# Kernel optimization log

Hardware: AMD Instinct MI355X
Metric: run time of the kernel (lower is better)

Reference implementation:

```python
import jax, jax.numpy as jnp
import numpy as np

N_HEAD = 12

def setup_inputs() -> dict:
    key = jax.random.key(0)
    ks = jax.random.split(key, 5)
    B, T, C = 4, 2048, 768
    x = jax.random.normal(ks[0], (B, T, C), dtype=jnp.float32)
    s_in = 1.0 / np.sqrt(C)
    W_qkv = jax.random.normal(ks[1], (C, 3 * C), dtype=jnp.float32) * s_in
    b_qkv = jnp.zeros((3 * C,), dtype=jnp.float32)
    W_proj = jax.random.normal(ks[2], (C, C), dtype=jnp.float32) * s_in
    b_proj = jnp.zeros((C,), dtype=jnp.float32)
    return {"x": x, "W_qkv": W_qkv, "b_qkv": b_qkv, "W_proj": W_proj, "b_proj": b_proj}


def reference(x, W_qkv, b_qkv, W_proj, b_proj):
    B, T, C = x.shape
    H = N_HEAD
    D = C // H  # head dim
    qkv = x @ W_qkv + b_qkv                      # [B,T,3C]
    q, k, v = jnp.split(qkv, 3, axis=-1)
    # [B,T,C] -> [B,H,T,D]
    q = q.reshape(B, T, H, D).transpose(0, 2, 1, 3)
    k = k.reshape(B, T, H, D).transpose(0, 2, 1, 3)
    v = v.reshape(B, T, H, D).transpose(0, 2, 1, 3)
    att = jnp.einsum("bhqd,bhkd->bhqk", q, k) / jnp.sqrt(jnp.asarray(D, x.dtype))
    causal = jnp.tril(jnp.ones((T, T), dtype=bool))
    att = jnp.where(causal, att, jnp.asarray(-jnp.inf, att.dtype))
    att = jax.nn.softmax(att, axis=-1)
    y = jnp.einsum("bhqk,bhkd->bhqd", att, v)    # [B,H,T,D]
    y = y.transpose(0, 2, 1, 3).reshape(B, T, C)
    return y @ W_proj + b_proj
```

## Files before the change

### kernel.cpp

```cpp
#include <hip/hip_runtime.h>
#include <hip/hip_bf16.h>

typedef __bf16 bf16x8 __attribute__((ext_vector_type(8)));
typedef float f32x4 __attribute__((ext_vector_type(4)));
typedef unsigned int u32x4 __attribute__((ext_vector_type(4)));
typedef unsigned int u32x2 __attribute__((ext_vector_type(2)));
typedef int i32x2 __attribute__((ext_vector_type(2)));
typedef unsigned short u16;
typedef unsigned long long u64;

#define WAITVM(n) asm volatile("s_waitcnt vmcnt(" #n ")" ::: "memory")
#define SBAR() asm volatile("s_barrier" ::: "memory")

__device__ __forceinline__ u16 f2bf(float f) {
  unsigned u = __builtin_bit_cast(unsigned, f);
  u += 0x7FFFu + ((u >> 16) & 1u);
  return (u16)(u >> 16);
}
__device__ __forceinline__ unsigned cvtpk(float a, float b) {
  float2 f; f.x = a; f.y = b;
  __hip_bfloat162 h = __float22bfloat162_rn(f);
  unsigned u;
  __builtin_memcpy(&u, &h, 4);
  return u;
}

__device__ __forceinline__ void plswap(unsigned &a, unsigned &b) {
  i32x2 r = __builtin_amdgcn_permlane32_swap((int)a, (int)b, false, false);
  a = (unsigned)r[0];
  b = (unsigned)r[1];
}

__device__ __forceinline__ void gll16(const u16* g, u16* l) {
  __builtin_amdgcn_global_load_lds(
      (const __attribute__((address_space(1))) unsigned int*)g,
      (__attribute__((address_space(3))) unsigned int*)l, 16, 0, 0);
}

__global__ void cast_x_kernel(const float* __restrict__ in, u16* __restrict__ out, int n4) {
  int i = blockIdx.x * blockDim.x + threadIdx.x;
  if (i >= n4) return;
  f32x4 v = *(const f32x4*)(in + (size_t)i * 4);
  u32x2 pk;
  pk[0] = cvtpk(v[0], v[1]);
  pk[1] = cvtpk(v[2], v[3]);
  *(u32x2*)(out + (size_t)i * 4) = pk;
}

__global__ void transpose_cast_kernel(const float* __restrict__ W, u16* __restrict__ WT, int K, int N) {
  __shared__ float tile[32][33];
  int c0 = blockIdx.x * 32, r0 = blockIdx.y * 32;
  int tx = threadIdx.x & 31, tg = threadIdx.x >> 5;
#pragma unroll
  for (int i = 0; i < 4; ++i) {
    int r = tg + i * 8;
    tile[r][tx] = W[(size_t)(r0 + r) * N + c0 + tx];
  }
  __syncthreads();
#pragma unroll
  for (int i = 0; i < 4; ++i) {
    int r = tg + i * 8;
    WT[(size_t)(c0 + r) * K + r0 + tx] = f2bf(tile[tx][r]);
  }
}

__global__ __launch_bounds__(256, 4) void gemm_qkv_kernel(
    const u16* __restrict__ A, const u16* __restrict__ BT, const float* __restrict__ bias,
    u16* __restrict__ Qb, u16* __restrict__ Kb, u16* __restrict__ Vt) {
  constexpr int K = 768;
  constexpr int NS = K / 32;
  __shared__ u16 Asm[2][128 * 32];
  __shared__ u16 Bsm[2][128 * 32];
  const int tid = threadIdx.x;
  const int w = tid >> 6, lane = tid & 63;
  const int l15 = lane & 15, quad = lane >> 4;
  const int srow = tid >> 2, scol = (tid & 3) * 8;
  const int m0 = blockIdx.y * 128, n0 = blockIdx.x * 128;
  const u16* Ag = A + (size_t)(m0 + srow) * K + scol;
  const u16* Bg = BT + (size_t)(n0 + srow) * K + scol;
  const int mw = (w >> 1) * 64, nw = (w & 1) * 64;
  f32x4 acc[4][4];
#pragma unroll
  for (int i = 0; i < 4; ++i)
#pragma unroll
    for (int j = 0; j < 4; ++j) acc[i][j] = {0.f, 0.f, 0.f, 0.f};

  auto STAGE = [&](int buf, int ks) {
    const u16* a = Ag + ks * 32;
    const u16* b = Bg + ks * 32;
#pragma unroll
    for (int rb = 0; rb < 2; ++rb) {
      gll16(a + (size_t)rb * 64 * K, &Asm[buf][(rb * 64 + w * 16) * 32]);
      gll16(b + (size_t)rb * 64 * K, &Bsm[buf][(rb * 64 + w * 16) * 32]);
    }
  };
  auto COMPUTE = [&](int buf) {
    bf16x8 af[4], bfj[4];
#pragma unroll
    for (int i = 0; i < 4; ++i) af[i] = *(const bf16x8*)&Asm[buf][(mw + i * 16 + l15) * 32 + quad * 8];
#pragma unroll
    for (int j = 0; j < 4; ++j) bfj[j] = *(const bf16x8*)&Bsm[buf][(nw + j * 16 + l15) * 32 + quad * 8];
#pragma unroll
    for (int i = 0; i < 4; ++i)
#pragma unroll
      for (int j = 0; j < 4; ++j)
        acc[i][j] = __builtin_amdgcn_mfma_f32_16x16x32_bf16(af[i], bfj[j], acc[i][j], 0, 0, 0);
  };

  STAGE(0, 0);
  for (int s = 0; s + 2 < NS; s += 2) {
    STAGE(1, s + 1); WAITVM(4); SBAR(); COMPUTE(0); SBAR();
    STAGE(0, s + 2); WAITVM(4); SBAR(); COMPUTE(1); SBAR();
  }
  STAGE(1, NS - 1); WAITVM(4); SBAR(); COMPUTE(0);
  WAITVM(0); SBAR(); COMPUTE(1);

  const int sec = blockIdx.x / 6;
  const int nbase = n0 - sec * 768;
#pragma unroll
  for (int j = 0; j < 4; ++j) {
    const int nloc = nbase + nw + j * 16 + l15;
    const float bv = bias[sec * 768 + nloc];
    const int h = nloc >> 6, d = nloc & 63;
#pragma unroll
    for (int i = 0; i < 4; ++i) {
      const int m = m0 + mw + i * 16 + quad * 4;
      const int bb = m >> 11, trow = m & 2047;
      if (sec == 2) {
        u32x2 pk;
        pk[0] = cvtpk(acc[i][j][0] + bv, acc[i][j][1] + bv);
        pk[1] = cvtpk(acc[i][j][2] + bv, acc[i][j][3] + bv);
        *(u32x2*)(Vt + (size_t)((bb * 12 + h) * 64 + d) * 2048 + trow) = pk;
      } else {
        u16* dst = (sec == 0) ? Qb : Kb;
        const float scl = (sec == 0) ? 0.125f * 1.44269504f : 1.0f;
#pragma unroll
        for (int r = 0; r < 4; ++r)
          dst[(size_t)((bb * 12 + h) * 2048 + trow + r) * 64 + d] = f2bf((acc[i][j][r] + bv) * scl);
      }
    }
  }
}

__global__ __launch_bounds__(256, 4) void gemm_proj_kernel(
    const u16* __restrict__ A, const u16* __restrict__ BT, const float* __restrict__ bias,
    float* __restrict__ out) {
  constexpr int K = 768;
  constexpr int NS = K / 32;
  __shared__ u16 Asm[2][64 * 32];
  __shared__ u16 Bsm[2][128 * 32];
  const int tid = threadIdx.x;
  const int w = tid >> 6, lane = tid & 63;
  const int l15 = lane & 15, quad = lane >> 4;
  const int srow = tid >> 2, scol = (tid & 3) * 8;
  const int m0 = blockIdx.y * 64, n0 = blockIdx.x * 128;
  const u16* Ag = A + (size_t)(m0 + srow) * K + scol;
  const u16* Bg = BT + (size_t)(n0 + srow) * K + scol;
  const int mw = (w >> 1) * 32, nw = (w & 1) * 64;
  f32x4 acc[2][4];
#pragma unroll
  for (int i = 0; i < 2; ++i)
#pragma unroll
    for (int j = 0; j < 4; ++j) acc[i][j] = {0.f, 0.f, 0.f, 0.f};

  auto STAGE = [&](int buf, int ks) {
    const u16* a = Ag + ks * 32;
    const u16* b = Bg + ks * 32;
    gll16(a, &Asm[buf][(w * 16) * 32]);
#pragma unroll
    for (int rb = 0; rb < 2; ++rb)
      gll16(b + (size_t)rb * 64 * K, &Bsm[buf][(rb * 64 + w * 16) * 32]);
  };
  auto COMPUTE = [&](int buf) {
    bf16x8 af[2], bfj[4];
#pragma unroll
    for (int i = 0; i < 2; ++i) af[i] = *(const bf16x8*)&Asm[buf][(mw + i * 16 + l15) * 32 + quad * 8];
#pragma unroll
    for (int j = 0; j < 4; ++j) bfj[j] = *(const bf16x8*)&Bsm[buf][(nw + j * 16 + l15) * 32 + quad * 8];
#pragma unroll
    for (int i = 0; i < 2; ++i)
#pragma unroll
      for (int j = 0; j < 4; ++j)
        acc[i][j] = __builtin_amdgcn_mfma_f32_16x16x32_bf16(af[i], bfj[j], acc[i][j], 0, 0, 0);
  };

  STAGE(0, 0);
  for (int s = 0; s + 2 < NS; s += 2) {
    STAGE(1, s + 1); WAITVM(3); SBAR(); COMPUTE(0); SBAR();
    STAGE(0, s + 2); WAITVM(3); SBAR(); COMPUTE(1); SBAR();
  }
  STAGE(1, NS - 1); WAITVM(3); SBAR(); COMPUTE(0);
  WAITVM(0); SBAR(); COMPUTE(1);

#pragma unroll
  for (int j = 0; j < 4; ++j) {
    const int n = n0 + nw + j * 16 + l15;
    const float bv = bias[n];
#pragma unroll
    for (int i = 0; i < 2; ++i) {
      const int m = m0 + mw + i * 16 + quad * 4;
#pragma unroll
      for (int r = 0; r < 4; ++r) out[(size_t)(m + r) * 768 + n] = acc[i][j][r] + bv;
    }
  }
}

__global__ __launch_bounds__(256) void attn_split_kernel(
    const u16* __restrict__ Qg, const u16* __restrict__ Kg, const u16* __restrict__ Vtg,
    u16* __restrict__ Yb, float* __restrict__ Opart, float* __restrict__ lpart) {
  constexpr int T = 2048, D = 64;
  constexpr int LDP = 72;
  constexpr float MBOUND = 20.0f;
  __shared__ u16 Ks[64 * LDP];
  __shared__ u16 VTs[64 * LDP];
  const int s = 79 - blockIdx.x;
  const int bh = blockIdx.y;
  int qt, c;
  if (s < 8) { qt = s; c = 0; }
  else if (s < 24) { qt = 8 + ((s - 8) >> 1); c = (s - 8) & 1; }
  else if (s < 48) { int u = s - 24; int q3 = u / 3; qt = 16 + q3; c = u - 3 * q3; }
  else { int u = s - 48; qt = 24 + (u >> 2); c = u & 3; }
  const int niter = min(8, qt + 1 - 8 * c);
  const int tid = threadIdx.x;
  const int w = tid >> 6, lane = tid & 63;
  const int l15 = lane & 15, quad = lane >> 4;
  const int srow = tid >> 2, scol = (tid & 3) * 16;
  const u16* Kp = Kg + (size_t)bh * T * D;
  const u16* VTp = Vtg + (size_t)bh * D * T;

  const int qq = qt * 64 + w * 16 + l15;
  const u16* qrow = Qg + ((size_t)bh * T + qq) * D;
  const bf16x8 qfa = *(const bf16x8*)(qrow + quad * 8);
  const bf16x8 qfb = *(const bf16x8*)(qrow + 32 + quad * 8);

  f32x4 o[4] = {{0,0,0,0},{0,0,0,0},{0,0,0,0},{0,0,0,0}};
  float lv = 0.f;

  int ktg = c * 8;
  u32x4 kA = *(const u32x4*)(Kp + (size_t)(ktg * 64 + srow) * D + scol);
  u32x4 kB = *(const u32x4*)(Kp + (size_t)(ktg * 64 + srow) * D + scol + 8);
  u32x4 vA = *(const u32x4*)(VTp + (size_t)srow * T + ktg * 64 + scol);
  u32x4 vB = *(const u32x4*)(VTp + (size_t)srow * T + ktg * 64 + scol + 8);

  for (int j = 0; j < niter; ++j) {
    ktg = c * 8 + j;
    __syncthreads();
    *(u32x4*)&Ks[srow * LDP + scol] = kA;
    *(u32x4*)&Ks[srow * LDP + scol + 8] = kB;
    {
      u32x2 t0; t0[0] = vA[0]; t0[1] = vA[1];
      u32x2 t1; t1[0] = vA[2]; t1[1] = vA[3];
      u32x2 t2; t2[0] = vB[0]; t2[1] = vB[1];
      u32x2 t3; t3[0] = vB[2]; t3[1] = vB[3];
      *(u32x2*)&VTs[srow * LDP + scol] = t0;
      *(u32x2*)&VTs[srow * LDP + scol + 8] = t1;
      *(u32x2*)&VTs[srow * LDP + scol + 4] = t2;
      *(u32x2*)&VTs[srow * LDP + scol + 12] = t3;
    }
    __syncthreads();
    if (j + 1 < niter) {
      const int k1 = (ktg + 1) * 64;
      kA = *(const u32x4*)(Kp + (size_t)(k1 + srow) * D + scol);
      kB = *(const u32x4*)(Kp + (size_t)(k1 + srow) * D + scol + 8);
      vA = *(const u32x4*)(VTp + (size_t)srow * T + k1 + scol);
      vB = *(const u32x4*)(VTp + (size_t)srow * T + k1 + scol + 8);
    }
    f32x4 sA[4];
#pragma unroll
    for (int t = 0; t < 4; ++t) sA[t] = {-MBOUND, -MBOUND, -MBOUND, -MBOUND};
#pragma unroll
    for (int t = 0; t < 4; ++t) {
      const bf16x8 kf0 = *(const bf16x8*)&Ks[(t * 16 + l15) * LDP + quad * 8];
      const bf16x8 kf1 = *(const bf16x8*)&Ks[(t * 16 + l15) * LDP + 32 + quad * 8];
      sA[t] = __builtin_amdgcn_mfma_f32_16x16x32_bf16(kf0, qfa, sA[t], 0, 0, 0);
      sA[t] = __builtin_amdgcn_mfma_f32_16x16x32_bf16(kf1, qfb, sA[t], 0, 0, 0);
    }
    if (ktg == qt) {
      const int k0 = ktg * 64;
#pragma unroll
      for (int t = 0; t < 4; ++t)
#pragma unroll
        for (int r = 0; r < 4; ++r)
          if (k0 + t * 16 + quad * 4 + r > qq) sA[t][r] = -1e30f;
    }
    unsigned W[4][2];
#pragma unroll
    for (int t = 0; t < 4; ++t) {
      float e0 = __builtin_amdgcn_exp2f(sA[t][0]);
      float e1 = __builtin_amdgcn_exp2f(sA[t][1]);
      float e2 = __builtin_amdgcn_exp2f(sA[t][2]);
      float e3 = __builtin_amdgcn_exp2f(sA[t][3]);
      lv += (e0 + e1) + (e2 + e3);
      W[t][0] = cvtpk(e0, e1);
      W[t][1] = cvtpk(e2, e3);
    }
    plswap(W[0][0], W[1][0]);
    plswap(W[0][1], W[1][1]);
    plswap(W[2][0], W[3][0]);
    plswap(W[2][1], W[3][1]);
    u32x4 paw; paw[0] = W[0][0]; paw[1] = W[0][1]; paw[2] = W[1][0]; paw[3] = W[1][1];
    u32x4 pbw; pbw[0] = W[2][0]; pbw[1] = W[2][1]; pbw[2] = W[3][0]; pbw[3] = W[3][1];
    const bf16x8 pa = __builtin_bit_cast(bf16x8, paw);
    const bf16x8 pb = __builtin_bit_cast(bf16x8, pbw);
#pragma unroll
    for (int t = 0; t < 4; ++t) {
      const bf16x8 vf0 = *(const bf16x8*)&VTs[(t * 16 + l15) * LDP + quad * 8];
      const bf16x8 vf1 = *(const bf16x8*)&VTs[(t * 16 + l15) * LDP + 32 + quad * 8];
      o[t] = __builtin_amdgcn_mfma_f32_16x16x32_bf16(vf0, pa, o[t], 0, 0, 0);
      o[t] = __builtin_amdgcn_mfma_f32_16x16x32_bf16(vf1, pb, o[t], 0, 0, 0);
    }
  }
  lv += __shfl_xor(lv, 16);
  lv += __shfl_xor(lv, 32);
  if (qt <= 7) {
    const float inv = 1.f / lv;
    const int bidx = bh / 12, hidx = bh % 12;
    u16* y = Yb + ((size_t)bidx * T + qq) * 768 + hidx * 64;
#pragma unroll
    for (int t = 0; t < 4; ++t) {
      u32x2 pk;
      pk[0] = cvtpk(o[t][0] * inv, o[t][1] * inv);
      pk[1] = cvtpk(o[t][2] * inv, o[t][3] * inv);
      *(u32x2*)(y + t * 16 + quad * 4) = pk;
    }
  } else {
    const size_t pidx = (size_t)bh * 80 + s;
    float* Op = Opart + pidx * 4096 + (size_t)(w * 16 + l15) * 64;
#pragma unroll
    for (int t = 0; t < 4; ++t) *(f32x4*)(Op + t * 16 + quad * 4) = o[t];
    if (quad == 0) lpart[pidx * 64 + w * 16 + l15] = lv;
  }
}

__global__ __launch_bounds__(256) void attn_combine_kernel(
    const float* __restrict__ Opart, const float* __restrict__ lpart, u16* __restrict__ Yb) {
  constexpr int T = 2048;
  const int qt = 8 + blockIdx.x;
  const int bh = blockIdx.y;
  const int nch = (qt < 16) ? 2 : (qt < 24) ? 3 : 4;
  const int off = (qt < 16) ? 8 + (qt - 8) * 2 : (qt < 24) ? 24 + (qt - 16) * 3 : 48 + (qt - 24) * 4;
  const size_t base = (size_t)bh * 80 + off;
  const int tid = threadIdx.x;
  const int q = tid >> 2, db = (tid & 3) * 16;
  f32x4 o[4] = {{0,0,0,0},{0,0,0,0},{0,0,0,0},{0,0,0,0}};
  float l = 0.f;
  for (int cc = 0; cc < nch; ++cc) {
    const float* Op = Opart + (base + cc) * 4096 + (size_t)q * 64 + db;
#pragma unroll
    for (int v = 0; v < 4; ++v) o[v] += *(const f32x4*)(Op + v * 4);
    l += lpart[(base + cc) * 64 + q];
  }
  const float inv = 1.f / l;
  const int bidx = bh / 12, hidx = bh % 12;
  u16* y = Yb + ((size_t)bidx * T + qt * 64 + q) * 768 + hidx * 64 + db;
  u32x4 pk;
  pk[0] = cvtpk(o[0][0] * inv, o[0][1] * inv);
  pk[1] = cvtpk(o[0][2] * inv, o[0][3] * inv);
  pk[2] = cvtpk(o[1][0] * inv, o[1][1] * inv);
  pk[3] = cvtpk(o[1][2] * inv, o[1][3] * inv);
  *(u32x4*)y = pk;
  pk[0] = cvtpk(o[2][0] * inv, o[2][1] * inv);
  pk[1] = cvtpk(o[2][2] * inv, o[2][3] * inv);
  pk[2] = cvtpk(o[3][0] * inv, o[3][1] * inv);
  pk[3] = cvtpk(o[3][2] * inv, o[3][3] * inv);
  *(u32x4*)(y + 8) = pk;
}

__global__ __launch_bounds__(256) void attn_kernel(
    const u16* __restrict__ Qg, const u16* __restrict__ Kg, const u16* __restrict__ Vtg,
    u16* __restrict__ Yb) {
  constexpr int T = 2048, D = 64;
  constexpr int LDP = 72;
  constexpr float MBOUND = 20.0f;
  __shared__ u16 Ks[64 * LDP];
  __shared__ u16 VTs[64 * LDP];
  __shared__ u16 Ps[4 * 32 * LDP];
  const int qb = 15 - blockIdx.x;
  const int bh = blockIdx.y;
  const int Q0 = qb * 128;
  const int bidx = bh / 12, hidx = bh % 12;
  const int tid = threadIdx.x;
  const int w = tid >> 6, lane = tid & 63;
  const int l15 = lane & 15, quad = lane >> 4;
  const int srow = tid >> 2, scol = (tid & 3) * 16;
  const u16* Kp = Kg + (size_t)bh * T * D;
  const u16* VTp = Vtg + (size_t)bh * D * T;
  u16* pw0 = &Ps[(w * 32) * LDP];
  u16* pw1 = &Ps[(w * 32 + 16) * LDP];
  const u16* qrow0 = Qg + ((size_t)bh * T + Q0 + w * 16 + l15) * D;
  const bf16x8 qf0a = *(const bf16x8*)(qrow0 + quad * 8);
  const bf16x8 qf0b = *(const bf16x8*)(qrow0 + 32 + quad * 8);
  const bf16x8 qf1a = *(const bf16x8*)(qrow0 + (size_t)64 * D + quad * 8);
  const bf16x8 qf1b = *(const bf16x8*)(qrow0 + (size_t)64 * D + 32 + quad * 8);
  const int qq0 = Q0 + w * 16 + l15, qq1 = qq0 + 64;
  f32x4 o0[4] = {{0,0,0,0},{0,0,0,0},{0,0,0,0},{0,0,0,0}};
  f32x4 o1[4] = {{0,0,0,0},{0,0,0,0},{0,0,0,0},{0,0,0,0}};
  float l0v = 0.f, l1v = 0.f;
  const int nkt = 2 * qb + 2;
  u32x4 kA = *(const u32x4*)(Kp + (size_t)srow * D + scol);
  u32x4 kB = *(const u32x4*)(Kp + (size_t)srow * D + scol + 8);
  u32x4 vA = *(const u32x4*)(VTp + (size_t)srow * T + scol);
  u32x4 vB = *(const u32x4*)(VTp + (size_t)srow * T + scol + 8);
  for (int kt = 0; kt < nkt; ++kt) {
    __syncthreads();
    *(u32x4*)&Ks[srow * LDP + scol] = kA;
    *(u32x4*)&Ks[srow * LDP + scol + 8] = kB;
    *(u32x4*)&VTs[srow * LDP + scol] = vA;
    *(u32x4*)&VTs[srow * LDP + scol + 8] = vB;
    __syncthreads();
    if (kt + 1 < nkt) {
      const int k1 = (kt + 1) * 64;
      kA = *(const u32x4*)(Kp + (size_t)(k1 + srow) * D + scol);
      kB = *(const u32x4*)(Kp + (size_t)(k1 + srow) * D + scol + 8);
      vA = *(const u32x4*)(VTp + (size_t)srow * T + k1 + scol);
      vB = *(const u32x4*)(VTp + (size_t)srow * T + k1 + scol + 8);
    }
    const int k0 = kt * 64;
    const bool g0a = (kt <= 2 * qb);
    f32x4 s0[4] = {{0,0,0,0},{0,0,0,0},{0,0,0,0},{0,0,0,0}};
    f32x4 s1[4] = {{0,0,0,0},{0,0,0,0},{0,0,0,0},{0,0,0,0}};
#pragma unroll
    for (int t = 0; t < 4; ++t) {
      const bf16x8 kf0 = *(const bf16x8*)&Ks[(t * 16 + l15) * LDP + quad * 8];
      const bf16x8 kf1 = *(const bf16x8*)&Ks[(t * 16 + l15) * LDP + 32 + quad * 8];
      s0[t] = __builtin_amdgcn_mfma_f32_16x16x32_bf16(kf0, qf0a, s0[t], 0, 0, 0);
      s0[t] = __builtin_amdgcn_mfma_f32_16x16x32_bf16(kf1, qf0b, s0[t], 0, 0, 0);
      s1[t] = __builtin_amdgcn_mfma_f32_16x16x32_bf16(kf0, qf1a, s1[t], 0, 0, 0);
      s1[t] = __builtin_amdgcn_mfma_f32_16x16x32_bf16(kf1, qf1b, s1[t], 0, 0, 0);
    }
    if (g0a) {
      if (kt == 2 * qb) {
#pragma unroll
        for (int t = 0; t < 4; ++t)
#pragma unroll
          for (int r = 0; r < 4; ++r)
            if (k0 + t * 16 + quad * 4 + r > qq0) s0[t][r] = -1e30f;
      }
#pragma unroll
      for (int t = 0; t < 4; ++t) {
        float e0 = __builtin_amdgcn_exp2f(s0[t][0] - MBOUND);
        float e1 = __builtin_amdgcn_exp2f(s0[t][1] - MBOUND);
        float e2 = __builtin_amdgcn_exp2f(s0[t][2] - MBOUND);
        float e3 = __builtin_amdgcn_exp2f(s0[t][3] - MBOUND);
        l0v += (e0 + e1) + (e2 + e3);
        u32x2 pk;
        pk[0] = cvtpk(e0, e1);
        pk[1] = cvtpk(e2, e3);
        *(u32x2*)&pw0[l15 * LDP + t * 16 + quad * 4] = pk;
      }
    }
    {
      if (kt == 2 * qb + 1) {
#pragma unroll
        for (int t = 0; t < 4; ++t)
#pragma unroll
          for (int r = 0; r < 4; ++r)
            if (k0 + t * 16 + quad * 4 + r > qq1) s1[t][r] = -1e30f;
      }
#pragma unroll
      for (int t = 0; t < 4; ++t) {
        float e0 = __builtin_amdgcn_exp2f(s1[t][0] - MBOUND);
        float e1 = __builtin_amdgcn_exp2f(s1[t][1] - MBOUND);
        float e2 = __builtin_amdgcn_exp2f(s1[t][2] - MBOUND);
        float e3 = __builtin_amdgcn_exp2f(s1[t][3] - MBOUND);
        l1v += (e0 + e1) + (e2 + e3);
        u32x2 pk;
        pk[0] = cvtpk(e0, e1);
        pk[1] = cvtpk(e2, e3);
        *(u32x2*)&pw1[l15 * LDP + t * 16 + quad * 4] = pk;
      }
    }
    const bf16x8 p0a = *(const bf16x8*)&pw0[l15 * LDP + quad * 8];
    const bf16x8 p0b = *(const bf16x8*)&pw0[l15 * LDP + 32 + quad * 8];
    const bf16x8 p1a = *(const bf16x8*)&pw1[l15 * LDP + quad * 8];
    const bf16x8 p1b = *(const bf16x8*)&pw1[l15 * LDP + 32 + quad * 8];
#pragma unroll
    for (int t = 0; t < 4; ++t) {
      const bf16x8 vf0 = *(const bf16x8*)&VTs[(t * 16 + l15) * LDP + quad * 8];
      const bf16x8 vf1 = *(const bf16x8*)&VTs[(t * 16 + l15) * LDP + 32 + quad * 8];
      if (g0a) {
        o0[t] = __builtin_amdgcn_mfma_f32_16x16x32_bf16(vf0, p0a, o0[t], 0, 0, 0);
        o0[t] = __builtin_amdgcn_mfma_f32_16x16x32_bf16(vf1, p0b, o0[t], 0, 0, 0);
      }
      o1[t] = __builtin_amdgcn_mfma_f32_16x16x32_bf16(vf0, p1a, o1[t], 0, 0, 0);
      o1[t] = __builtin_amdgcn_mfma_f32_16x16x32_bf16(vf1, p1b, o1[t], 0, 0, 0);
    }
  }
  l0v += __shfl_xor(l0v, 16); l0v += __shfl_xor(l0v, 32);
  l1v += __shfl_xor(l1v, 16); l1v += __shfl_xor(l1v, 32);
  const float inv0 = 1.f / l0v, inv1 = 1.f / l1v;
  u16* y0 = Yb + ((size_t)bidx * T + qq0) * 768 + hidx * 64;
  u16* y1 = Yb + ((size_t)bidx * T + qq1) * 768 + hidx * 64;
#pragma unroll
  for (int t = 0; t < 4; ++t) {
    u32x2 pk0, pk1;
    pk0[0] = cvtpk(o0[t][0] * inv0, o0[t][1] * inv0);
    pk0[1] = cvtpk(o0[t][2] * inv0, o0[t][3] * inv0);
    pk1[0] = cvtpk(o1[t][0] * inv1, o1[t][1] * inv1);
    pk1[1] = cvtpk(o1[t][2] * inv1, o1[t][3] * inv1);
    *(u32x2*)(y0 + t * 16 + quad * 4) = pk0;
    *(u32x2*)(y1 + t * 16 + quad * 4) = pk1;
  }
}

extern "C" void kernel_launch(void* const* d_in, const int* in_sizes, int n_in,
                              void* d_out, int out_size, void* d_ws, size_t ws_size,
                              hipStream_t stream) {
  const float* x = (const float*)d_in[0];
  const float* W_qkv = (const float*)d_in[1];
  const float* b_qkv = (const float*)d_in[2];
  const float* W_proj = (const float*)d_in[3];
  const float* b_proj = (const float*)d_in[4];
  float* out = (float*)d_out;

  constexpr size_t MC = (size_t)8192 * 768;
  u16* xb = (u16*)d_ws;
  u16* Qb = xb + MC;
  u16* Kb = Qb + MC;
  u16* Vt = Kb + MC;
  u16* Yb = Vt + MC;
  u16* WqkvT = Yb + MC;
  u16* WprojT = WqkvT + (size_t)2304 * 768;
  constexpr size_t BASE_U16 = 5 * MC + (size_t)2304 * 768 + (size_t)768 * 768;
  float* Opart = (float*)((u16*)d_ws + BASE_U16);
  float* lpart = Opart + (size_t)3840 * 4096;
  constexpr size_t NEED = BASE_U16 * 2 + ((size_t)3840 * 4096 + (size_t)3840 * 64) * 4;
  const bool use_split = (ws_size >= NEED);

  cast_x_kernel<<<6291456 / (4 * 256), 256, 0, stream>>>(x, xb, 6291456 / 4);
  transpose_cast_kernel<<<dim3(2304 / 32, 768 / 32), 256, 0, stream>>>(W_qkv, WqkvT, 768, 2304);
  transpose_cast_kernel<<<dim3(768 / 32, 768 / 32), 256, 0, stream>>>(W_proj, WprojT, 768, 768);
  gemm_qkv_kernel<<<dim3(18, 64), 256, 0, stream>>>(xb, WqkvT, b_qkv, Qb, Kb, Vt);
  if (use_split) {
    attn_split_kernel<<<dim3(80, 48), 256, 0, stream>>>(Qb, Kb, Vt, Yb, Opart, lpart);
    attn_combine_kernel<<<dim3(24, 48), 256, 0, stream>>>(Opart, lpart, Yb);
  } else {
    attn_kernel<<<dim3(16, 48), 256, 0, stream>>>(Qb, Kb, Vt, Yb);
  }
  gemm_proj_kernel<<<dim3(6, 128), 256, 0, stream>>>(Yb, WprojT, b_proj, out);
}
```

Measured before the change: 229.2 us.

## Process two query tiles per split attention block to reuse K/V loads

Each split-attention block now handles 128 query rows (two 64-row tiles) and shares every K/V tile staged in LDS between both, halving K/V global traffic and LDS staging per query. The grid, partial buffers and combine kernel are rebuilt around 128-row tiles, and the combine kernel now handles 128 rows per block. s_setprio hints are added around the MFMA sections. In exchange the grid has half as many blocks, register pressure rises from two accumulator sets, and the first tile does masked or skipped work on the diagonal iterations.

After: 238.5 us. +4.0%, slower.

```diff
diff --git a/kernel.cpp b/kernel.cpp
--- a/kernel.cpp
+++ b/kernel.cpp
@@ -213,14 +213,15 @@
   constexpr float MBOUND = 20.0f;
   __shared__ u16 Ks[64 * LDP];
   __shared__ u16 VTs[64 * LDP];
-  const int s = 79 - blockIdx.x;
+  const int s = 39 - blockIdx.x;
   const int bh = blockIdx.y;
-  int qt, c;
-  if (s < 8) { qt = s; c = 0; }
-  else if (s < 24) { qt = 8 + ((s - 8) >> 1); c = (s - 8) & 1; }
-  else if (s < 48) { int u = s - 24; int q3 = u / 3; qt = 16 + q3; c = u - 3 * q3; }
-  else { int u = s - 48; qt = 24 + (u >> 2); c = u & 3; }
-  const int niter = min(8, qt + 1 - 8 * c);
+  int qt2, c;
+  if (s < 4) { qt2 = s; c = 0; }
+  else if (s < 12) { qt2 = 4 + ((s - 4) >> 1); c = (s - 4) & 1; }
+  else if (s < 24) { int u = s - 12; int q3 = u / 3; qt2 = 8 + q3; c = u - 3 * q3; }
+  else { int u = s - 24; qt2 = 12 + (u >> 2); c = u & 3; }
+  const int nkt = 2 * qt2 + 2;
+  const int niter = min(8, nkt - 8 * c);
   const int tid = threadIdx.x;
   const int w = tid >> 6, lane = tid & 63;
   const int l15 = lane & 15, quad = lane >> 4;
@@ -228,13 +229,17 @@
   const u16* Kp = Kg + (size_t)bh * T * D;
   const u16* VTp = Vtg + (size_t)bh * D * T;
 
-  const int qq = qt * 64 + w * 16 + l15;
-  const u16* qrow = Qg + ((size_t)bh * T + qq) * D;
-  const bf16x8 qfa = *(const bf16x8*)(qrow + quad * 8);
-  const bf16x8 qfb = *(const bf16x8*)(qrow + 32 + quad * 8);
-
-  f32x4 o[4] = {{0,0,0,0},{0,0,0,0},{0,0,0,0},{0,0,0,0}};
-  float lv = 0.f;
+  const int Q0 = qt2 * 128;
+  const int qq0 = Q0 + w * 16 + l15, qq1 = qq0 + 64;
+  const u16* qrow = Qg + ((size_t)bh * T + qq0) * D;
+  const bf16x8 qf0a = *(const bf16x8*)(qrow + quad * 8);
+  const bf16x8 qf0b = *(const bf16x8*)(qrow + 32 + quad * 8);
+  const bf16x8 qf1a = *(const bf16x8*)(qrow + (size_t)64 * D + quad * 8);
+  const bf16x8 qf1b = *(const bf16x8*)(qrow + (size_t)64 * D + 32 + quad * 8);
+
+  f32x4 o0[4] = {{0,0,0,0},{0,0,0,0},{0,0,0,0},{0,0,0,0}};
+  f32x4 o1[4] = {{0,0,0,0},{0,0,0,0},{0,0,0,0},{0,0,0,0}};
+  float lv0 = 0.f, lv1 = 0.f;
 
   int ktg = c * 8;
   u32x4 kA = *(const u32x4*)(Kp + (size_t)(ktg * 64 + srow) * D + scol);
@@ -265,105 +270,171 @@
       vA = *(const u32x4*)(VTp + (size_t)srow * T + k1 + scol);
       vB = *(const u32x4*)(VTp + (size_t)srow * T + k1 + scol + 8);
     }
-    f32x4 sA[4];
-#pragma unroll
-    for (int t = 0; t < 4; ++t) sA[t] = {-MBOUND, -MBOUND, -MBOUND, -MBOUND};
-#pragma unroll
-    for (int t = 0; t < 4; ++t) {
-      const bf16x8 kf0 = *(const bf16x8*)&Ks[(t * 16 + l15) * LDP + quad * 8];
-      const bf16x8 kf1 = *(const bf16x8*)&Ks[(t * 16 + l15) * LDP + 32 + quad * 8];
-      sA[t] = __builtin_amdgcn_mfma_f32_16x16x32_bf16(kf0, qfa, sA[t], 0, 0, 0);
-      sA[t] = __builtin_amdgcn_mfma_f32_16x16x32_bf16(kf1, qfb, sA[t], 0, 0, 0);
-    }
-    if (ktg == qt) {
-      const int k0 = ktg * 64;
-#pragma unroll
-      for (int t = 0; t < 4; ++t)
-#pragma unroll
-        for (int r = 0; r < 4; ++r)
-          if (k0 + t * 16 + quad * 4 + r > qq) sA[t][r] = -1e30f;
-    }
-    unsigned W[4][2];
-#pragma unroll
-    for (int t = 0; t < 4; ++t) {
-      float e0 = __builtin_amdgcn_exp2f(sA[t][0]);
-      float e1 = __builtin_amdgcn_exp2f(sA[t][1]);
-      float e2 = __builtin_amdgcn_exp2f(sA[t][2]);
-      float e3 = __builtin_amdgcn_exp2f(sA[t][3]);
-      lv += (e0 + e1) + (e2 + e3);
-      W[t][0] = cvtpk(e0, e1);
-      W[t][1] = cvtpk(e2, e3);
-    }
-    plswap(W[0][0], W[1][0]);
-    plswap(W[0][1], W[1][1]);
-    plswap(W[2][0], W[3][0]);
-    plswap(W[2][1], W[3][1]);
-    u32x4 paw; paw[0] = W[0][0]; paw[1] = W[0][1]; paw[2] = W[1][0]; paw[3] = W[1][1];
-    u32x4 pbw; pbw[0] = W[2][0]; pbw[1] = W[2][1]; pbw[2] = W[3][0]; pbw[3] = W[3][1];
-    const bf16x8 pa = __builtin_bit_cast(bf16x8, paw);
-    const bf16x8 pb = __builtin_bit_cast(bf16x8, pbw);
+    const bool g0a = (ktg <= 2 * qt2);
+    const int k0 = ktg * 64;
+    bf16x8 pa0, pb0, pa1, pb1;
+    if (g0a) {
+      f32x4 sA[4];
+#pragma unroll
+      for (int t = 0; t < 4; ++t) sA[t] = {-MBOUND, -MBOUND, -MBOUND, -MBOUND};
+      __builtin_amdgcn_s_setprio(1);
+#pragma unroll
+      for (int t = 0; t < 4; ++t) {
+        const bf16x8 kf0 = *(const bf16x8*)&Ks[(t * 16 + l15) * LDP + quad * 8];
+        const bf16x8 kf1 = *(const bf16x8*)&Ks[(t * 16 + l15) * LDP + 32 + quad * 8];
+        sA[t] = __builtin_amdgcn_mfma_f32_16x16x32_bf16(kf0, qf0a, sA[t], 0, 0, 0);
+        sA[t] = __builtin_amdgcn_mfma_f32_16x16x32_bf16(kf1, qf0b, sA[t], 0, 0, 0);
+      }
+      __builtin_amdgcn_s_setprio(0);
+      if (ktg == 2 * qt2) {
+#pragma unroll
+        for (int t = 0; t < 4; ++t)
+#pragma unroll
+          for (int r = 0; r < 4; ++r)
+            if (k0 + t * 16 + quad * 4 + r > qq0) sA[t][r] = -1e30f;
+      }
+      unsigned W[4][2];
+#pragma unroll
+      for (int t = 0; t < 4; ++t) {
+        float e0 = __builtin_amdgcn_exp2f(sA[t][0]);
+        float e1 = __builtin_amdgcn_exp2f(sA[t][1]);
+        float e2 = __builtin_amdgcn_exp2f(sA[t][2]);
+        float e3 = __builtin_amdgcn_exp2f(sA[t][3]);
+        lv0 += (e0 + e1) + (e2 + e3);
+        W[t][0] = cvtpk(e0, e1);
+        W[t][1] = cvtpk(e2, e3);
+      }
+      plswap(W[0][0], W[1][0]);
+      plswap(W[0][1], W[1][1]);
+      plswap(W[2][0], W[3][0]);
+      plswap(W[2][1], W[3][1]);
+      u32x4 paw; paw[0] = W[0][0]; paw[1] = W[0][1]; paw[2] = W[1][0]; paw[3] = W[1][1];
+      u32x4 pbw; pbw[0] = W[2][0]; pbw[1] = W[2][1]; pbw[2] = W[3][0]; pbw[3] = W[3][1];
+      pa0 = __builtin_bit_cast(bf16x8, paw);
+      pb0 = __builtin_bit_cast(bf16x8, pbw);
+    }
+    {
+      f32x4 sA[4];
+#pragma unroll
+      for (int t = 0; t < 4; ++t) sA[t] = {-MBOUND, -MBOUND, -MBOUND, -MBOUND};
+      __builtin_amdgcn_s_setprio(1);
+#pragma unroll
+      for (int t = 0; t < 4; ++t) {
+        const bf16x8 kf0 = *(const bf16x8*)&Ks[(t * 16 + l15) * LDP + quad * 8];
+        const bf16x8 kf1 = *(const bf16x8*)&Ks[(t * 16 + l15) * LDP + 32 + quad * 8];
+        sA[t] = __builtin_amdgcn_mfma_f32_16x16x32_bf16(kf0, qf1a, sA[t], 0, 0, 0);
+        sA[t] = __builtin_amdgcn_mfma_f32_16x16x32_bf16(kf1, qf1b, sA[t], 0, 0, 0);
+      }
+      __builtin_amdgcn_s_setprio(0);
+      if (ktg == 2 * qt2 + 1) {
+#pragma unroll
+        for (int t = 0; t < 4; ++t)
+#pragma unroll
+          for (int r = 0; r < 4; ++r)
+            if (k0 + t * 16 + quad * 4 + r > qq1) sA[t][r] = -1e30f;
+      }
+      unsigned W[4][2];
+#pragma unroll
+      for (int t = 0; t < 4; ++t) {
+        float e0 = __builtin_amdgcn_exp2f(sA[t][0]);
+        float e1 = __builtin_amdgcn_exp2f(sA[t][1]);
+        float e2 = __builtin_amdgcn_exp2f(sA[t][2]);
+        float e3 = __builtin_amdgcn_exp2f(sA[t][3]);
+        lv1 += (e0 + e1) + (e2 + e3);
+        W[t][0] = cvtpk(e0, e1);
+        W[t][1] = cvtpk(e2, e3);
+      }
+      plswap(W[0][0], W[1][0]);
+      plswap(W[0][1], W[1][1]);
+      plswap(W[2][0], W[3][0]);
+      plswap(W[2][1], W[3][1]);
+      u32x4 paw; paw[0] = W[0][0]; paw[1] = W[0][1]; paw[2] = W[1][0]; paw[3] = W[1][1];
+      u32x4 pbw; pbw[0] = W[2][0]; pbw[1] = W[2][1]; pbw[2] = W[3][0]; pbw[3] = W[3][1];
+      pa1 = __builtin_bit_cast(bf16x8, paw);
+      pb1 = __builtin_bit_cast(bf16x8, pbw);
+    }
+    __builtin_amdgcn_s_setprio(1);
 #pragma unroll
     for (int t = 0; t < 4; ++t) {
       const bf16x8 vf0 = *(const bf16x8*)&VTs[(t * 16 + l15) * LDP + quad * 8];
       const bf16x8 vf1 = *(const bf16x8*)&VTs[(t * 16 + l15) * LDP + 32 + quad * 8];
-      o[t] = __builtin_amdgcn_mfma_f32_16x16x32_bf16(vf0, pa, o[t], 0, 0, 0);
-      o[t] = __builtin_amdgcn_mfma_f32_16x16x32_bf16(vf1, pb, o[t], 0, 0, 0);
-    }
-  }
-  lv += __shfl_xor(lv, 16);
-  lv += __shfl_xor(lv, 32);
-  if (qt <= 7) {
-    const float inv = 1.f / lv;
+      if (g0a) {
+        o0[t] = __builtin_amdgcn_mfma_f32_16x16x32_bf16(vf0, pa0, o0[t], 0, 0, 0);
+        o0[t] = __builtin_amdgcn_mfma_f32_16x16x32_bf16(vf1, pb0, o0[t], 0, 0, 0);
+      }
+      o1[t] = __builtin_amdgcn_mfma_f32_16x16x32_bf16(vf0, pa1, o1[t], 0, 0, 0);
+      o1[t] = __builtin_amdgcn_mfma_f32_16x16x32_bf16(vf1, pb1, o1[t], 0, 0, 0);
+    }
+    __builtin_amdgcn_s_setprio(0);
+  }
+  lv0 += __shfl_xor(lv0, 16); lv0 += __shfl_xor(lv0, 32);
+  lv1 += __shfl_xor(lv1, 16); lv1 += __shfl_xor(lv1, 32);
+  if (qt2 <= 3) {
+    const float inv0 = 1.f / lv0, inv1 = 1.f / lv1;
     const int bidx = bh / 12, hidx = bh % 12;
-    u16* y = Yb + ((size_t)bidx * T + qq) * 768 + hidx * 64;
+    u16* y0 = Yb + ((size_t)bidx * T + qq0) * 768 + hidx * 64;
+    u16* y1 = Yb + ((size_t)bidx * T + qq1) * 768 + hidx * 64;
 #pragma unroll
     for (int t = 0; t < 4; ++t) {
-      u32x2 pk;
-      pk[0] = cvtpk(o[t][0] * inv, o[t][1] * inv);
-      pk[1] = cvtpk(o[t][2] * inv, o[t][3] * inv);
-      *(u32x2*)(y + t * 16 + quad * 4) = pk;
+      u32x2 pk0, pk1;
+      pk0[0] = cvtpk(o0[t][0] * inv0, o0[t][1] * inv0);
+      pk0[1] = cvtpk(o0[t][2] * inv0, o0[t][3] * inv0);
+      pk1[0] = cvtpk(o1[t][0] * inv1, o1[t][1] * inv1);
+      pk1[1] = cvtpk(o1[t][2] * inv1, o1[t][3] * inv1);
+      *(u32x2*)(y0 + t * 16 + quad * 4) = pk0;
+      *(u32x2*)(y1 + t * 16 + quad * 4) = pk1;
     }
   } else {
-    const size_t pidx = (size_t)bh * 80 + s;
-    float* Op = Opart + pidx * 4096 + (size_t)(w * 16 + l15) * 64;
-#pragma unroll
-    for (int t = 0; t < 4; ++t) *(f32x4*)(Op + t * 16 + quad * 4) = o[t];
-    if (quad == 0) lpart[pidx * 64 + w * 16 + l15] = lv;
+    const size_t pidx = (size_t)bh * 40 + s;
+    float* Op0 = Opart + pidx * 8192 + (size_t)(w * 16 + l15) * 64;
+    float* Op1 = Op0 + (size_t)64 * 64;
+#pragma unroll
+    for (int t = 0; t < 4; ++t) {
+      *(f32x4*)(Op0 + t * 16 + quad * 4) = o0[t];
+      *(f32x4*)(Op1 + t * 16 + quad * 4) = o1[t];
+    }
+    if (quad == 0) {
+      lpart[pidx * 128 + w * 16 + l15] = lv0;
+      lpart[pidx * 128 + 64 + w * 16 + l15] = lv1;
+    }
   }
 }
 
 __global__ __launch_bounds__(256) void attn_combine_kernel(
     const float* __restrict__ Opart, const float* __restrict__ lpart, u16* __restrict__ Yb) {
   constexpr int T = 2048;
-  const int qt = 8 + blockIdx.x;
+  const int qt2 = 4 + blockIdx.x;
   const int bh = blockIdx.y;
-  const int nch = (qt < 16) ? 2 : (qt < 24) ? 3 : 4;
-  const int off = (qt < 16) ? 8 + (qt - 8) * 2 : (qt < 24) ? 24 + (qt - 16) * 3 : 48 + (qt - 24) * 4;
-  const size_t base = (size_t)bh * 80 + off;
+  const int nch = (qt2 < 8) ? 2 : (qt2 < 12) ? 3 : 4;
+  const int off = (qt2 < 8) ? 4 + (qt2 - 4) * 2 : (qt2 < 12) ? 12 + (qt2 - 8) * 3 : 24 + (qt2 - 12) * 4;
+  const size_t base = (size_t)bh * 40 + off;
   const int tid = threadIdx.x;
-  const int q = tid >> 2, db = (tid & 3) * 16;
-  f32x4 o[4] = {{0,0,0,0},{0,0,0,0},{0,0,0,0},{0,0,0,0}};
+  const int q = tid >> 1, db = (tid & 1) * 32;
+  f32x4 o[8] = {{0,0,0,0},{0,0,0,0},{0,0,0,0},{0,0,0,0},{0,0,0,0},{0,0,0,0},{0,0,0,0},{0,0,0,0}};
   float l = 0.f;
   for (int cc = 0; cc < nch; ++cc) {
-    const float* Op = Opart + (base + cc) * 4096 + (size_t)q * 64 + db;
-#pragma unroll
-    for (int v = 0; v < 4; ++v) o[v] += *(const f32x4*)(Op + v * 4);
-    l += lpart[(base + cc) * 64 + q];
+    const float* Op = Opart + (base + cc) * 8192 + (size_t)q * 64 + db;
+#pragma unroll
+    for (int v = 0; v < 8; ++v) o[v] += *(const f32x4*)(Op + v * 4);
+    l += lpart[(base + cc) * 128 + q];
   }
   const float inv = 1.f / l;
   const int bidx = bh / 12, hidx = bh % 12;
-  u16* y = Yb + ((size_t)bidx * T + qt * 64 + q) * 768 + hidx * 64 + db;
-  u32x4 pk;
-  pk[0] = cvtpk(o[0][0] * inv, o[0][1] * inv);
-  pk[1] = cvtpk(o[0][2] * inv, o[0][3] * inv);
-  pk[2] = cvtpk(o[1][0] * inv, o[1][1] * inv);
-  pk[3] = cvtpk(o[1][2] * inv, o[1][3] * inv);
-  *(u32x4*)y = pk;
-  pk[0] = cvtpk(o[2][0] * inv, o[2][1] * inv);
-  pk[1] = cvtpk(o[2][2] * inv, o[2][3] * inv);
-  pk[2] = cvtpk(o[3][0] * inv, o[3][1] * inv);
-  pk[3] = cvtpk(o[3][2] * inv, o[3][3] * inv);
-  *(u32x4*)(y + 8) = pk;
+  u16* y = Yb + ((size_t)bidx * T + qt2 * 128 + q) * 768 + hidx * 64 + db;
+#pragma unroll
+  for (int g = 0; g < 2; ++g) {
+    u32x4 pk;
+    pk[0] = cvtpk(o[g * 4 + 0][0] * inv, o[g * 4 + 0][1] * inv);
+    pk[1] = cvtpk(o[g * 4 + 0][2] * inv, o[g * 4 + 0][3] * inv);
+    pk[2] = cvtpk(o[g * 4 + 1][0] * inv, o[g * 4 + 1][1] * inv);
+    pk[3] = cvtpk(o[g * 4 + 1][2] * inv, o[g * 4 + 1][3] * inv);
+    *(u32x4*)(y + g * 16) = pk;
+    pk[0] = cvtpk(o[g * 4 + 2][0] * inv, o[g * 4 + 2][1] * inv);
+    pk[1] = cvtpk(o[g * 4 + 2][2] * inv, o[g * 4 + 2][3] * inv);
+    pk[2] = cvtpk(o[g * 4 + 3][0] * inv, o[g * 4 + 3][1] * inv);
+    pk[3] = cvtpk(o[g * 4 + 3][2] * inv, o[g * 4 + 3][3] * inv);
+    *(u32x4*)(y + g * 16 + 8) = pk;
+  }
 }
 
 __global__ __launch_bounds__(256) void attn_kernel(
@@ -523,8 +594,8 @@
   u16* WprojT = WqkvT + (size_t)2304 * 768;
   constexpr size_t BASE_U16 = 5 * MC + (size_t)2304 * 768 + (size_t)768 * 768;
   float* Opart = (float*)((u16*)d_ws + BASE_U16);
-  float* lpart = Opart + (size_t)3840 * 4096;
-  constexpr size_t NEED = BASE_U16 * 2 + ((size_t)3840 * 4096 + (size_t)3840 * 64) * 4;
+  float* lpart = Opart + (size_t)1920 * 8192;
+  constexpr size_t NEED = BASE_U16 * 2 + ((size_t)1920 * 8192 + (size_t)1920 * 128) * 4;
   const bool use_split = (ws_size >= NEED);
 
   cast_x_kernel<<<6291456 / (4 * 256), 256, 0, stream>>>(x, xb, 6291456 / 4);
@@ -532,8 +603,8 @@
   transpose_cast_kernel<<<dim3(768 / 32, 768 / 32), 256, 0, stream>>>(W_proj, WprojT, 768, 768);
   gemm_qkv_kernel<<<dim3(18, 64), 256, 0, stream>>>(xb, WqkvT, b_qkv, Qb, Kb, Vt);
   if (use_split) {
-    attn_split_kernel<<<dim3(80, 48), 256, 0, stream>>>(Qb, Kb, Vt, Yb, Opart, lpart);
-    attn_combine_kernel<<<dim3(24, 48), 256, 0, stream>>>(Opart, lpart, Yb);
+    attn_split_kernel<<<dim3(40, 48), 256, 0, stream>>>(Qb, Kb, Vt, Yb, Opart, lpart);
+    attn_combine_kernel<<<dim3(12, 48), 256, 0, stream>>>(Opart, lpart, Yb);
   } else {
     attn_kernel<<<dim3(16, 48), 256, 0, stream>>>(Qb, Kb, Vt, Yb);
   }
```

## Double-buffer K/V tiles in LDS and compute softmax row sums via MFMA

Applied to the files above, without the earlier changes.

Moves the attention split kernel's K/V staging to two LDS buffers. The next tile is written to the alternate buffer after the current compute, which cuts the loop from two barriers per iteration to one. Row sums of the exponentials now come from an MFMA against a vector of ones instead of scalar adds plus cross-lane shuffles. s_setprio hints are placed around the MFMA sections. This doubles LDS use per block, which may lower occupancy, and adds two MFMAs per iteration.

After: 227.4 us. No clear change (-0.8%).

```diff
diff --git a/kernel.cpp b/kernel.cpp
--- a/kernel.cpp
+++ b/kernel.cpp
@@ -211,8 +211,8 @@
   constexpr int T = 2048, D = 64;
   constexpr int LDP = 72;
   constexpr float MBOUND = 20.0f;
-  __shared__ u16 Ks[64 * LDP];
-  __shared__ u16 VTs[64 * LDP];
+  __shared__ u16 Ks[2][64 * LDP];
+  __shared__ u16 VTs[2][64 * LDP];
   const int s = 79 - blockIdx.x;
   const int bh = blockIdx.y;
   int qt, c;
@@ -233,48 +233,53 @@
   const bf16x8 qfa = *(const bf16x8*)(qrow + quad * 8);
   const bf16x8 qfb = *(const bf16x8*)(qrow + 32 + quad * 8);
 
+  u32x4 onesw; onesw[0] = 0x3F803F80u; onesw[1] = 0x3F803F80u; onesw[2] = 0x3F803F80u; onesw[3] = 0x3F803F80u;
+  const bf16x8 ones = __builtin_bit_cast(bf16x8, onesw);
+
   f32x4 o[4] = {{0,0,0,0},{0,0,0,0},{0,0,0,0},{0,0,0,0}};
-  float lv = 0.f;
-
-  int ktg = c * 8;
-  u32x4 kA = *(const u32x4*)(Kp + (size_t)(ktg * 64 + srow) * D + scol);
-  u32x4 kB = *(const u32x4*)(Kp + (size_t)(ktg * 64 + srow) * D + scol + 8);
-  u32x4 vA = *(const u32x4*)(VTp + (size_t)srow * T + ktg * 64 + scol);
-  u32x4 vB = *(const u32x4*)(VTp + (size_t)srow * T + ktg * 64 + scol + 8);
+  f32x4 lacc = {0.f, 0.f, 0.f, 0.f};
+
+  u32x4 kA, kB, vA, vB;
+  auto LOADT = [&](int kt) {
+    const int k1 = kt * 64;
+    kA = *(const u32x4*)(Kp + (size_t)(k1 + srow) * D + scol);
+    kB = *(const u32x4*)(Kp + (size_t)(k1 + srow) * D + scol + 8);
+    vA = *(const u32x4*)(VTp + (size_t)srow * T + k1 + scol);
+    vB = *(const u32x4*)(VTp + (size_t)srow * T + k1 + scol + 8);
+  };
+  auto STORET = [&](int buf) {
+    *(u32x4*)&Ks[buf][srow * LDP + scol] = kA;
+    *(u32x4*)&Ks[buf][srow * LDP + scol + 8] = kB;
+    u32x2 t0; t0[0] = vA[0]; t0[1] = vA[1];
+    u32x2 t1; t1[0] = vA[2]; t1[1] = vA[3];
+    u32x2 t2; t2[0] = vB[0]; t2[1] = vB[1];
+    u32x2 t3; t3[0] = vB[2]; t3[1] = vB[3];
+    *(u32x2*)&VTs[buf][srow * LDP + scol] = t0;
+    *(u32x2*)&VTs[buf][srow * LDP + scol + 8] = t1;
+    *(u32x2*)&VTs[buf][srow * LDP + scol + 4] = t2;
+    *(u32x2*)&VTs[buf][srow * LDP + scol + 12] = t3;
+  };
+
+  LOADT(c * 8);
+  STORET(0);
+  if (niter > 1) LOADT(c * 8 + 1);
+  __syncthreads();
 
   for (int j = 0; j < niter; ++j) {
-    ktg = c * 8 + j;
-    __syncthreads();
-    *(u32x4*)&Ks[srow * LDP + scol] = kA;
-    *(u32x4*)&Ks[srow * LDP + scol + 8] = kB;
-    {
-      u32x2 t0; t0[0] = vA[0]; t0[1] = vA[1];
-      u32x2 t1; t1[0] = vA[2]; t1[1] = vA[3];
-      u32x2 t2; t2[0] = vB[0]; t2[1] = vB[1];
-      u32x2 t3; t3[0] = vB[2]; t3[1] = vB[3];
-      *(u32x2*)&VTs[srow * LDP + scol] = t0;
-      *(u32x2*)&VTs[srow * LDP + scol + 8] = t1;
-      *(u32x2*)&VTs[srow * LDP + scol + 4] = t2;
-      *(u32x2*)&VTs[srow * LDP + scol + 12] = t3;
-    }
-    __syncthreads();
-    if (j + 1 < niter) {
-      const int k1 = (ktg + 1) * 64;
-      kA = *(const u32x4*)(Kp + (size_t)(k1 + srow) * D + scol);
-      kB = *(const u32x4*)(Kp + (size_t)(k1 + srow) * D + scol + 8);
-      vA = *(const u32x4*)(VTp + (size_t)srow * T + k1 + scol);
-      vB = *(const u32x4*)(VTp + (size_t)srow * T + k1 + scol + 8);
-    }
+    const int buf = j & 1;
+    const int ktg = c * 8 + j;
     f32x4 sA[4];
 #pragma unroll
     for (int t = 0; t < 4; ++t) sA[t] = {-MBOUND, -MBOUND, -MBOUND, -MBOUND};
+    __builtin_amdgcn_s_setprio(1);
 #pragma unroll
     for (int t = 0; t < 4; ++t) {
-      const bf16x8 kf0 = *(const bf16x8*)&Ks[(t * 16 + l15) * LDP + quad * 8];
-      const bf16x8 kf1 = *(const bf16x8*)&Ks[(t * 16 + l15) * LDP + 32 + quad * 8];
+      const bf16x8 kf0 = *(const bf16x8*)&Ks[buf][(t * 16 + l15) * LDP + quad * 8];
+      const bf16x8 kf1 = *(const bf16x8*)&Ks[buf][(t * 16 + l15) * LDP + 32 + quad * 8];
       sA[t] = __builtin_amdgcn_mfma_f32_16x16x32_bf16(kf0, qfa, sA[t], 0, 0, 0);
       sA[t] = __builtin_amdgcn_mfma_f32_16x16x32_bf16(kf1, qfb, sA[t], 0, 0, 0);
     }
+    __builtin_amdgcn_s_setprio(0);
     if (ktg == qt) {
       const int k0 = ktg * 64;
 #pragma unroll
@@ -290,7 +295,6 @@
       float e1 = __builtin_amdgcn_exp2f(sA[t][1]);
       float e2 = __builtin_amdgcn_exp2f(sA[t][2]);
       float e3 = __builtin_amdgcn_exp2f(sA[t][3]);
-      lv += (e0 + e1) + (e2 + e3);
       W[t][0] = cvtpk(e0, e1);
       W[t][1] = cvtpk(e2, e3);
     }
@@ -302,16 +306,25 @@
     u32x4 pbw; pbw[0] = W[2][0]; pbw[1] = W[2][1]; pbw[2] = W[3][0]; pbw[3] = W[3][1];
     const bf16x8 pa = __builtin_bit_cast(bf16x8, paw);
     const bf16x8 pb = __builtin_bit_cast(bf16x8, pbw);
+    __builtin_amdgcn_s_setprio(1);
+    lacc = __builtin_amdgcn_mfma_f32_16x16x32_bf16(ones, pa, lacc, 0, 0, 0);
+    lacc = __builtin_amdgcn_mfma_f32_16x16x32_bf16(ones, pb, lacc, 0, 0, 0);
 #pragma unroll
     for (int t = 0; t < 4; ++t) {
-      const bf16x8 vf0 = *(const bf16x8*)&VTs[(t * 16 + l15) * LDP + quad * 8];
-      const bf16x8 vf1 = *(const bf16x8*)&VTs[(t * 16 + l15) * LDP + 32 + quad * 8];
+      const bf16x8 vf0 = *(const bf16x8*)&VTs[buf][(t * 16 + l15) * LDP + quad * 8];
+      const bf16x8 vf1 = *(const bf16x8*)&VTs[buf][(t * 16 + l15) * LDP + 32 + quad * 8];
       o[t] = __builtin_amdgcn_mfma_f32_16x16x32_bf16(vf0, pa, o[t], 0, 0, 0);
       o[t] = __builtin_amdgcn_mfma_f32_16x16x32_bf16(vf1, pb, o[t], 0, 0, 0);
     }
-  }
-  lv += __shfl_xor(lv, 16);
-  lv += __shfl_xor(lv, 32);
+    __builtin_amdgcn_s_setprio(0);
+    if (j + 1 < niter) {
+      STORET(buf ^ 1);
+      if (j + 2 < niter) LOADT(c * 8 + j + 2);
+    }
+    __syncthreads();
+  }
+
+  const float lv = lacc[0];
   if (qt <= 7) {
     const float inv = 1.f / lv;
     const int bidx = bh / 12, hidx = bh % 12;
```
